# Kernel optimization log

Hardware: AMD Instinct MI355X
Metric: run time of the kernel (lower is better)

Reference implementation:

```python
import jax, jax.numpy as jnp
import numpy as np

D = 256  # input_dim


def setup_inputs() -> dict:
    key = jax.random.key(0)
    ks = jax.random.split(key, 10)
    s = 1.0 / np.sqrt(D)  # torch Linear init scale (uniform bound)
    desc0 = jax.random.normal(ks[0], (4, 4096, D), dtype=jnp.float32)
    desc1 = jax.random.normal(ks[1], (4, 4096, D), dtype=jnp.float32)
    def lin(kw, kb):
        W = jax.random.uniform(kw, (D, D), jnp.float32, -s, s)
        b = jax.random.uniform(kb, (D,), jnp.float32, -s, s)
        return W, b
    Wq, bq = lin(ks[2], ks[3])
    Wk, bk = lin(ks[4], ks[5])
    Wv, bv = lin(ks[6], ks[7])
    Wo, bo = lin(ks[8], ks[9])
    return {"desc0": desc0, "desc1": desc1,
            "Wq": Wq, "bq": bq, "Wk": Wk, "bk": bk,
            "Wv": Wv, "bv": bv, "Wo": Wo, "bo": bo}


def reference(desc0, desc1, Wq, bq, Wk, bk, Wv, bv, Wo, bo):
    # torch Linear: y = x @ W.T + b
    q = desc0 @ Wq.T + bq                      # [B, N0, D]
    k = desc1 @ Wk.T + bk                      # [B, N1, D]
    v = desc1 @ Wv.T + bv                      # [B, N1, D]
    scale = 1.0 / jnp.sqrt(jnp.asarray(q.shape[-1], q.dtype))
    attn = jnp.einsum('bqd,bkd->bqk', q, k) * scale  # [B, N0, N1]
    weights = jax.nn.softmax(attn, axis=-1)
    out = jnp.einsum('bqk,bkd->bqd', weights, v)     # [B, N0, D]
    return out @ Wo.T + bo
```

## Files before the change

### kernel.cpp

```cpp
#include <hip/hip_runtime.h>


typedef __attribute__((ext_vector_type(8))) __bf16 bf16x8;
typedef __attribute__((ext_vector_type(4))) float f32x4;
typedef __attribute__((ext_vector_type(16))) float f32x16;
typedef __attribute__((ext_vector_type(4))) unsigned int u32x4;
typedef __attribute__((ext_vector_type(2))) unsigned int u32x2;
typedef __attribute__((ext_vector_type(4))) unsigned short us16x4;

__device__ __forceinline__ unsigned short f2bf(float f) {
  unsigned u = __builtin_bit_cast(unsigned, f);
  u += 0x7FFFu + ((u >> 16) & 1u);
  return (unsigned short)(u >> 16);
}
__device__ __forceinline__ unsigned pk2(float a, float b) {
  return (unsigned)f2bf(a) | ((unsigned)f2bf(b) << 16);
}
__device__ __forceinline__ unsigned cvtpk(float lo, float hi) {
  unsigned r;
  asm("v_cvt_pk_bf16_f32 %0, %1, %2" : "=v"(r) : "v"(lo), "v"(hi));
  return r;
}
__device__ __forceinline__ float bf2f(unsigned short s) {
  return __builtin_bit_cast(float, ((unsigned)s) << 16);
}
__device__ __forceinline__ int swz4(int r) { return (r ^ (r >> 2)) & 3; }
__device__ __forceinline__ bf16x8 ldbf16(const void* p) {
  return __builtin_bit_cast(bf16x8, *(const u32x4*)p);
}
__device__ __forceinline__ f32x4 mfma16(bf16x8 a, bf16x8 b, f32x4 c) {
  return __builtin_amdgcn_mfma_f32_16x16x32_bf16(a, b, c, 0, 0, 0);
}
__device__ __forceinline__ f32x16 mfma32(bf16x8 a, bf16x8 b, f32x16 c) {
  return __builtin_amdgcn_mfma_f32_32x32x16_bf16(a, b, c, 0, 0, 0);
}
__device__ __forceinline__ void gld16(void* lds, const void* gsrc) {
  __builtin_amdgcn_global_load_lds(
      (const __attribute__((address_space(1))) unsigned int*)gsrc,
      (__attribute__((address_space(3))) unsigned int*)lds, 16, 0, 0);
}

template <int IN_BF16, int MODE>
__global__ __launch_bounds__(256, 4) void proj_k(const void* __restrict__ Ain,
                                                 const float* __restrict__ W,
                                                 const float* __restrict__ bias,
                                                 void* __restrict__ Cout) {
  __shared__ __align__(16) unsigned short Al[2][64 * 32];
  __shared__ __align__(16) unsigned short Wl[2][64 * 32];
  __shared__ float biasl[64];
  const int tid = threadIdx.x;
  const int w = tid >> 6, l = tid & 63, g = l >> 4, c = l & 15;
  const int mt = blockIdx.x & 255, nq = blockIdx.x >> 8;
  const int row0 = mt * 64, n0 = nq * 64;
  if (tid < 64) biasl[tid] = bias[n0 + tid];

  const int sr = tid >> 2, seg = tid & 3;
  const int ssw = swz4(sr);

  {
    if (IN_BF16) {
      const unsigned short* ap = (const unsigned short*)Ain + (size_t)(row0 + sr) * 256 + seg * 8;
      *(u32x4*)&Al[0][sr * 32 + ((seg ^ ssw) << 3)] = *(const u32x4*)ap;
    } else {
      const float* ap = (const float*)Ain + (size_t)(row0 + sr) * 256 + seg * 8;
      float4 x = *(const float4*)ap, y = *(const float4*)(ap + 4);
      u32x4 v; v[0] = pk2(x.x, x.y); v[1] = pk2(x.z, x.w); v[2] = pk2(y.x, y.y); v[3] = pk2(y.z, y.w);
      *(u32x4*)&Al[0][sr * 32 + ((seg ^ ssw) << 3)] = v;
    }
    const float* wp = W + (size_t)(n0 + sr) * 256 + seg * 8;
    float4 x = *(const float4*)wp, y = *(const float4*)(wp + 4);
    u32x4 v; v[0] = pk2(x.x, x.y); v[1] = pk2(x.z, x.w); v[2] = pk2(y.x, y.y); v[3] = pk2(y.z, y.w);
    *(u32x4*)&Wl[0][sr * 32 + ((seg ^ ssw) << 3)] = v;
  }
  __syncthreads();

  f32x4 acc[4];
#pragma unroll
  for (int jt = 0; jt < 4; ++jt) acc[jt] = (f32x4){0.f, 0.f, 0.f, 0.f};

#pragma unroll 1
  for (int ch = 0; ch < 8; ++ch) {
    const int cur = ch & 1;
    const bool pre = (ch + 1 < 8);
    float4 ax, ay, wx, wy; u32x4 abv;
    if (pre) {
      const int ko = (ch + 1) * 32 + seg * 8;
      if (IN_BF16) {
        abv = *(const u32x4*)((const unsigned short*)Ain + (size_t)(row0 + sr) * 256 + ko);
      } else {
        const float* ap = (const float*)Ain + (size_t)(row0 + sr) * 256 + ko;
        ax = *(const float4*)ap; ay = *(const float4*)(ap + 4);
      }
      const float* wp = W + (size_t)(n0 + sr) * 256 + ko;
      wx = *(const float4*)wp; wy = *(const float4*)(wp + 4);
    }
    const int ra = w * 16 + c;
    bf16x8 af = ldbf16(&Al[cur][ra * 32 + ((g ^ swz4(ra)) << 3)]);
#pragma unroll
    for (int jt = 0; jt < 4; ++jt) {
      const int j = jt * 16 + c;
      bf16x8 bfr = ldbf16(&Wl[cur][j * 32 + ((g ^ swz4(j)) << 3)]);
      acc[jt] = mfma16(af, bfr, acc[jt]);
    }
    if (pre) {
      u32x4 v;
      if (IN_BF16) v = abv;
      else { v[0] = pk2(ax.x, ax.y); v[1] = pk2(ax.z, ax.w); v[2] = pk2(ay.x, ay.y); v[3] = pk2(ay.z, ay.w); }
      *(u32x4*)&Al[1 - cur][sr * 32 + ((seg ^ ssw) << 3)] = v;
      u32x4 vw; vw[0] = pk2(wx.x, wx.y); vw[1] = pk2(wx.z, wx.w); vw[2] = pk2(wy.x, wy.y); vw[3] = pk2(wy.z, wy.w);
      *(u32x4*)&Wl[1 - cur][sr * 32 + ((seg ^ ssw) << 3)] = vw;
    }
    __syncthreads();
  }

#pragma unroll
  for (int jt = 0; jt < 4; ++jt) {
    const int col = n0 + jt * 16 + c;
    const float bv = biasl[jt * 16 + c];
    const int rloc = w * 16 + (g << 2);
    if (MODE == 0) {
      unsigned short* q = (unsigned short*)Cout;
#pragma unroll
      for (int r = 0; r < 4; ++r)
        q[(size_t)(row0 + rloc + r) * 256 + col] = f2bf(acc[jt][r] + bv);
    } else if (MODE == 1) {
      unsigned short* vt = (unsigned short*)Cout;
      const int n = row0 + rloc;
      const int b = n >> 12, nl = n & 4095;
      us16x4 pk;
      pk[0] = f2bf(acc[jt][0] + bv); pk[1] = f2bf(acc[jt][1] + bv);
      pk[2] = f2bf(acc[jt][2] + bv); pk[3] = f2bf(acc[jt][3] + bv);
      *(us16x4*)(vt + (size_t)b * 1048576 + (size_t)(nl >> 6) * 16384 + col * 64 + (nl & 63)) = pk;
    } else {
      float* o = (float*)Cout;
#pragma unroll
      for (int r = 0; r < 4; ++r)
        o[(size_t)(row0 + rloc + r) * 256 + col] = acc[jt][r] + bv;
    }
  }
}

template <int NS>
__global__ __launch_bounds__(512, 2) void attn_k(const unsigned short* __restrict__ qg,
                                                 const unsigned short* __restrict__ kg,
                                                 const unsigned short* __restrict__ vg,
                                                 unsigned short* __restrict__ part,
                                                 float* __restrict__ lw) {
  __shared__ __align__(16) unsigned char smem[148480];
  const int tid = threadIdx.x, w = tid >> 6, l = tid & 63;
  const int l31 = l & 31, h5 = l >> 5;
  const int qt = w >> 1, hf = w & 1;
  const int bid = blockIdx.x;
  const int b4 = bid & 3;
  const int s = (NS == 2) ? ((bid >> 2) & 1) : 0;
  const int qtl = (NS == 2) ? (bid >> 3) : (bid >> 2);
  const int q0 = qtl * 128;
  const int NT = (NS == 2) ? 32 : 64;

  const unsigned short* kb = kg + (size_t)b4 * 1048576 + (size_t)s * 524288;
  const unsigned short* vb = vg + (size_t)b4 * 1048576 + (size_t)s * 32 * 16384;

  bf16x8 qf[16];
  {
    const unsigned short* qp = qg + ((size_t)b4 * 4096 + q0 + qt * 32 + l31) * 256;
#pragma unroll
    for (int kst = 0; kst < 16; ++kst) qf[kst] = ldbf16(qp + kst * 16 + h5 * 8);
  }

  f32x16 o[4];
#pragma unroll
  for (int d = 0; d < 4; ++d)
#pragma unroll
    for (int r = 0; r < 16; ++r) o[d][r] = 0.f;
  float l_run = 0.f;

  int goffK[4], goffV[4];
#pragma unroll
  for (int i = 0; i < 4; ++i) {
    const int sl = i * 512 + tid;
    const int kk = sl >> 5, ch = sl & 31;
    goffK[i] = kk * 256 + ((ch ^ (kk & 31)) << 3);
    const int r = sl >> 4, p16 = sl & 15;
    const int x = p16 ^ (r & 15);
    goffV[i] = (2 * r + (x >> 3)) * 64 + ((x & 7) << 3);
  }
#define STAGE(buf, t1)                                                                   \
  {                                                                                      \
    const unsigned short* _ks = kb + (size_t)(t1) * 16384;                               \
    const unsigned short* _vs = vb + (size_t)(t1) * 16384;                               \
    _Pragma("unroll") for (int i = 0; i < 4; ++i)                                        \
        gld16(smem + (buf) * 32768 + i * 8192 + w * 1024, _ks + goffK[i]);               \
    _Pragma("unroll") for (int i = 0; i < 4; ++i)                                        \
        gld16(smem + 65536 + (buf) * 32768 + i * 8192 + w * 1024, _vs + goffV[i]);       \
  }

  STAGE(0, 0);
  __syncthreads();

  const float alpha = 0.09016844f;
  unsigned char* Pq = smem + 131072 + qt * 4096;
  const int kkr = hf * 32 + l31;

#pragma unroll 1
  for (int t = 0; t < NT; ++t) {
    const int cur = t & 1;
    if (t + 1 < NT) STAGE(1 - cur, t + 1);

    const unsigned char* Kc = smem + cur * 32768 + kkr * 512;
    f32x16 sa, sb;
#pragma unroll
    for (int r = 0; r < 16; ++r) { sa[r] = 0.f; sb[r] = 0.f; }
    __builtin_amdgcn_s_setprio(1);
#pragma unroll
    for (int kst = 0; kst < 16; ++kst) {
      bf16x8 kf = ldbf16(Kc + (((kst * 2 + h5) ^ l31) << 4));
      if (kst & 1) sb = mfma32(kf, qf[kst], sb);
      else         sa = mfma32(kf, qf[kst], sa);
    }
    __builtin_amdgcn_s_setprio(0);

    float p[16];
#pragma unroll
    for (int r = 0; r < 16; ++r) p[r] = exp2f((sa[r] + sb[r]) * alpha);
    float ls = ((p[0] + p[1]) + (p[2] + p[3])) + ((p[4] + p[5]) + (p[6] + p[7])) +
               (((p[8] + p[9]) + (p[10] + p[11])) + ((p[12] + p[13]) + (p[14] + p[15])));
    ls += __shfl_xor(ls, 32);
    l_run += ls;

    unsigned u[8];
#pragma unroll
    for (int i = 0; i < 8; ++i) u[i] = cvtpk(p[2 * i], p[2 * i + 1]);
#pragma unroll
    for (int j = 0; j < 4; ++j) {
      u32x2 dv; dv[0] = u[2 * j]; dv[1] = u[2 * j + 1];
      *(u32x2*)(Pq + l31 * 128 + (((j + 4 * hf) ^ (l31 & 7)) << 4) + h5 * 8) = dv;
    }

    asm volatile("s_waitcnt lgkmcnt(0)\n\ts_barrier" ::: "memory");
    __builtin_amdgcn_sched_barrier(0);

    bf16x8 pb[4];
#pragma unroll
    for (int kst = 0; kst < 4; ++kst)
      pb[kst] = ldbf16(Pq + l31 * 128 + (((kst * 2 + h5) ^ (l31 & 7)) << 4));
    const unsigned char* Vc = smem + 65536 + cur * 32768;
    __builtin_amdgcn_s_setprio(1);
#pragma unroll
    for (int dsub = 0; dsub < 4; ++dsub) {
      const int dm = hf * 128 + dsub * 32 + l31;
      const int r = dm >> 1;
      const unsigned char* Vr = Vc + r * 256;
      const int xb = (dm & 1) * 8;
#pragma unroll
      for (int kst = 0; kst < 4; ++kst) {
        bf16x8 vf = ldbf16(Vr + (((xb + kst * 2 + h5) ^ (r & 15)) << 4));
        o[dsub] = mfma32(vf, pb[kst], o[dsub]);
      }
    }
    __builtin_amdgcn_s_setprio(0);

    __syncthreads();
  }
#undef STAGE

  float* Lb = (float*)(smem + 147456);
  if (l < 32) Lb[(qt * 2 + hf) * 32 + l31] = l_run;
  __syncthreads();

  unsigned char* T = smem + w * 16384;
#pragma unroll
  for (int dsub = 0; dsub < 4; ++dsub)
#pragma unroll
    for (int rg = 0; rg < 4; ++rg) {
      f32x4 wv;
      wv[0] = o[dsub][4 * rg + 0]; wv[1] = o[dsub][4 * rg + 1];
      wv[2] = o[dsub][4 * rg + 2]; wv[3] = o[dsub][4 * rg + 3];
      const int d4 = dsub * 8 + rg * 2 + h5;
      *(f32x4*)(T + l31 * 512 + ((d4 ^ l31) << 4)) = wv;
    }
  asm volatile("s_waitcnt lgkmcnt(0)" ::: "memory");
  __builtin_amdgcn_sched_barrier(0);
  {
    const int q2 = l >> 1, dh = l & 1;
    unsigned short* op = part + (size_t)s * 4194304 +
                         ((size_t)b4 * 4096 + q0 + qt * 32 + q2) * 256 + hf * 128 + dh * 64;
#pragma unroll
    for (int jj = 0; jj < 8; ++jj) {
      f32x4 r0 = *(const f32x4*)(T + q2 * 512 + (((dh * 16 + 2 * jj) ^ q2) << 4));
      f32x4 r1 = *(const f32x4*)(T + q2 * 512 + (((dh * 16 + 2 * jj + 1) ^ q2) << 4));
      u32x4 ov;
      ov[0] = pk2(r0[0], r0[1]); ov[1] = pk2(r0[2], r0[3]);
      ov[2] = pk2(r1[0], r1[1]); ov[3] = pk2(r1[2], r1[3]);
      *(u32x4*)(op + jj * 8) = ov;
    }
  }
  if (hf == 0 && l < 32) {
    const float lt = Lb[(qt * 2) * 32 + l31] + Lb[(qt * 2 + 1) * 32 + l31];
    lw[(size_t)s * 16384 + (size_t)b4 * 4096 + q0 + qt * 32 + l31] = lt;
  }
}

__global__ __launch_bounds__(256, 8) void merge_k(unsigned short* __restrict__ part,
                                                  const float* __restrict__ lw, int ns) {
  const int idx = blockIdx.x * 256 + threadIdx.x;
  const int q = idx >> 5, d8 = (idx & 31) * 8;
  unsigned short* p0 = part + (size_t)q * 256 + d8;
  u32x4 a = *(const u32x4*)p0;
  float acc[8];
#pragma unroll
  for (int i = 0; i < 4; ++i) {
    acc[2 * i] = bf2f((unsigned short)(a[i] & 0xFFFF));
    acc[2 * i + 1] = bf2f((unsigned short)(a[i] >> 16));
  }
  float lt = lw[q];
  if (ns == 2) {
    u32x4 b = *(const u32x4*)(p0 + 4194304);
#pragma unroll
    for (int i = 0; i < 4; ++i) {
      acc[2 * i] += bf2f((unsigned short)(b[i] & 0xFFFF));
      acc[2 * i + 1] += bf2f((unsigned short)(b[i] >> 16));
    }
    lt += lw[16384 + q];
  }
  const float inv = 1.f / lt;
  u32x4 ov;
#pragma unroll
  for (int i = 0; i < 4; ++i) ov[i] = pk2(acc[2 * i] * inv, acc[2 * i + 1] * inv);
  *(u32x4*)p0 = ov;
}

extern "C" void kernel_launch(void* const* d_in, const int* in_sizes, int n_in,
                              void* d_out, int out_size, void* d_ws, size_t ws_size,
                              hipStream_t stream) {
  (void)in_sizes; (void)n_in; (void)out_size;
  const float* desc0 = (const float*)d_in[0];
  const float* desc1 = (const float*)d_in[1];
  const float* Wq = (const float*)d_in[2];
  const float* bq = (const float*)d_in[3];
  const float* Wk = (const float*)d_in[4];
  const float* bk = (const float*)d_in[5];
  const float* Wv = (const float*)d_in[6];
  const float* bv = (const float*)d_in[7];
  const float* Wo = (const float*)d_in[8];
  const float* bo = (const float*)d_in[9];

  unsigned char* ws = (unsigned char*)d_ws;
  unsigned short* qw = (unsigned short*)(ws);
  unsigned short* kw = (unsigned short*)(ws + 8388608);
  unsigned short* vw = (unsigned short*)(ws + 16777216);
  unsigned short* part = (unsigned short*)(ws + 25165824);
  float* lwp = (float*)(ws + 41943040);

  const bool two = (ws_size >= 42008576ull);

  proj_k<0, 0><<<1024, 256, 0, stream>>>(desc0, Wq, bq, qw);
  proj_k<0, 0><<<1024, 256, 0, stream>>>(desc1, Wk, bk, kw);
  proj_k<0, 1><<<1024, 256, 0, stream>>>(desc1, Wv, bv, vw);
  if (two) {
    attn_k<2><<<256, 512, 0, stream>>>(qw, kw, vw, part, lwp);
    merge_k<<<2048, 256, 0, stream>>>(part, lwp, 2);
  } else {
    lwp = (float*)(ws + 33554432);
    attn_k<1><<<128, 512, 0, stream>>>(qw, kw, vw, part, lwp);
    merge_k<<<2048, 256, 0, stream>>>(part, lwp, 1);
  }
  proj_k<1, 2><<<1024, 256, 0, stream>>>(part, Wo, bo, (float*)d_out);
}
```

Before: 135.4 us.

## Pre-swizzle K into MFMA fragment layout and load it directly to registers

The K projection now writes its output in a fragment-ordered layout, so each attention wave can load its K operands straight from global memory into registers. This drops K from shared memory: no LDS staging, no swizzled LDS reads, and a smaller LDS footprint. The next tile's K is prefetched into registers during the current iteration. In exchange each wave carries 16 extra vector registers of K, and the coalesced K load from global memory sits on the critical path, which could add register pressure or latency.

```diff
diff --git a/kernel.cpp b/kernel.cpp
--- a/kernel.cpp
+++ b/kernel.cpp
@@ -131,22 +131,32 @@
       pk[0] = f2bf(acc[jt][0] + bv); pk[1] = f2bf(acc[jt][1] + bv);
       pk[2] = f2bf(acc[jt][2] + bv); pk[3] = f2bf(acc[jt][3] + bv);
       *(us16x4*)(vt + (size_t)b * 1048576 + (size_t)(nl >> 6) * 16384 + col * 64 + (nl & 63)) = pk;
-    } else {
+    } else if (MODE == 2) {
       float* o = (float*)Cout;
 #pragma unroll
       for (int r = 0; r < 4; ++r)
         o[(size_t)(row0 + rloc + r) * 256 + col] = acc[jt][r] + bv;
+    } else {
+      unsigned short* kq = (unsigned short*)Cout;
+      const int kst = (n0 >> 4) + jt;
+      const int j = c & 7, hb = c >> 3;
+#pragma unroll
+      for (int r = 0; r < 4; ++r) {
+        const int n = row0 + rloc + r;
+        kq[(size_t)(n >> 5) * 8192 + kst * 512 + (((n & 31) + hb * 32) << 3) + j] =
+            f2bf(acc[jt][r] + bv);
+      }
     }
   }
 }
 
 template <int NS>
 __global__ __launch_bounds__(512, 2) void attn_k(const unsigned short* __restrict__ qg,
-                                                 const unsigned short* __restrict__ kg,
+                                                 const unsigned short* __restrict__ kfb,
                                                  const unsigned short* __restrict__ vg,
                                                  unsigned short* __restrict__ part,
                                                  float* __restrict__ lw) {
-  __shared__ __align__(16) unsigned char smem[148480];
+  __shared__ __align__(16) unsigned char smem[132096];
   const int tid = threadIdx.x, w = tid >> 6, l = tid & 63;
   const int l31 = l & 31, h5 = l >> 5;
   const int qt = w >> 1, hf = w & 1;
@@ -157,7 +167,7 @@
   const int q0 = qtl * 128;
   const int NT = (NS == 2) ? 32 : 64;
 
-  const unsigned short* kb = kg + (size_t)b4 * 1048576 + (size_t)s * 524288;
+  const unsigned short* kb = kfb + (size_t)b4 * 1048576 + (size_t)s * 524288;
   const unsigned short* vb = vg + (size_t)b4 * 1048576 + (size_t)s * 32 * 16384;
 
   bf16x8 qf[16];
@@ -174,48 +184,49 @@
     for (int r = 0; r < 16; ++r) o[d][r] = 0.f;
   float l_run = 0.f;
 
-  int goffK[4], goffV[4];
+  int goffV[4];
 #pragma unroll
   for (int i = 0; i < 4; ++i) {
     const int sl = i * 512 + tid;
-    const int kk = sl >> 5, ch = sl & 31;
-    goffK[i] = kk * 256 + ((ch ^ (kk & 31)) << 3);
     const int r = sl >> 4, p16 = sl & 15;
     const int x = p16 ^ (r & 15);
     goffV[i] = (2 * r + (x >> 3)) * 64 + ((x & 7) << 3);
   }
-#define STAGE(buf, t1)                                                                   \
-  {                                                                                      \
-    const unsigned short* _ks = kb + (size_t)(t1) * 16384;                               \
-    const unsigned short* _vs = vb + (size_t)(t1) * 16384;                               \
-    _Pragma("unroll") for (int i = 0; i < 4; ++i)                                        \
-        gld16(smem + (buf) * 32768 + i * 8192 + w * 1024, _ks + goffK[i]);               \
-    _Pragma("unroll") for (int i = 0; i < 4; ++i)                                        \
-        gld16(smem + 65536 + (buf) * 32768 + i * 8192 + w * 1024, _vs + goffV[i]);       \
-  }
-
-  STAGE(0, 0);
+#define STAGEV(buf, t1)                                                            \
+  {                                                                                \
+    const unsigned short* _vs = vb + (size_t)(t1) * 16384;                         \
+    _Pragma("unroll") for (int i = 0; i < 4; ++i)                                  \
+        gld16(smem + (buf) * 32768 + i * 8192 + w * 1024, _vs + goffV[i]);         \
+  }
+#define LOADK(dst, t1)                                                             \
+  {                                                                                \
+    const unsigned short* _tb = kb + (size_t)((t1) * 2 + hf) * 8192 + l * 8;       \
+    _Pragma("unroll") for (int kst = 0; kst < 16; ++kst)                           \
+        dst[kst] = *(const u32x4*)(_tb + kst * 512);                               \
+  }
+
+  u32x4 kf[16];
+  LOADK(kf, 0);
+  STAGEV(0, 0);
   __syncthreads();
 
   const float alpha = 0.09016844f;
-  unsigned char* Pq = smem + 131072 + qt * 4096;
-  const int kkr = hf * 32 + l31;
+  unsigned char* Pq = smem + 65536 + qt * 4096;
 
 #pragma unroll 1
   for (int t = 0; t < NT; ++t) {
     const int cur = t & 1;
-    if (t + 1 < NT) STAGE(1 - cur, t + 1);
-
-    const unsigned char* Kc = smem + cur * 32768 + kkr * 512;
+    if (t + 1 < NT) STAGEV(1 - cur, t + 1);
+
     f32x16 sa, sb;
 #pragma unroll
     for (int r = 0; r < 16; ++r) { sa[r] = 0.f; sb[r] = 0.f; }
     __builtin_amdgcn_s_setprio(1);
 #pragma unroll
     for (int kst = 0; kst < 16; ++kst) {
-      bf16x8 kf = ldbf16(Kc + (((kst * 2 + h5) ^ l31) << 4));
-      if (kst & 1) sb = mfma32(kf, qf[kst], sb);
-      else         sa = mfma32(kf, qf[kst], sa);
+      bf16x8 kfr = __builtin_bit_cast(bf16x8, kf[kst]);
+      if (kst & 1) sb = mfma32(kfr, qf[kst], sb);
+      else         sa = mfma32(kfr, qf[kst], sa);
     }
     __builtin_amdgcn_s_setprio(0);
 
@@ -236,6 +247,8 @@
       *(u32x2*)(Pq + l31 * 128 + (((j + 4 * hf) ^ (l31 & 7)) << 4) + h5 * 8) = dv;
     }
 
+    if (t + 1 < NT) LOADK(kf, t + 1);
+
     asm volatile("s_waitcnt lgkmcnt(0)\n\ts_barrier" ::: "memory");
     __builtin_amdgcn_sched_barrier(0);
 
@@ -243,7 +256,7 @@
 #pragma unroll
     for (int kst = 0; kst < 4; ++kst)
       pb[kst] = ldbf16(Pq + l31 * 128 + (((kst * 2 + h5) ^ (l31 & 7)) << 4));
-    const unsigned char* Vc = smem + 65536 + cur * 32768;
+    const unsigned char* Vc = smem + cur * 32768;
     __builtin_amdgcn_s_setprio(1);
 #pragma unroll
     for (int dsub = 0; dsub < 4; ++dsub) {
@@ -261,9 +274,10 @@
 
     __syncthreads();
   }
-#undef STAGE
-
-  float* Lb = (float*)(smem + 147456);
+#undef STAGEV
+#undef LOADK
+
+  float* Lb = (float*)(smem + 131072);
   if (l < 32) Lb[(qt * 2 + hf) * 32 + l31] = l_run;
   __syncthreads();
 
@@ -354,7 +368,7 @@
   const bool two = (ws_size >= 42008576ull);
 
   proj_k<0, 0><<<1024, 256, 0, stream>>>(desc0, Wq, bq, qw);
-  proj_k<0, 0><<<1024, 256, 0, stream>>>(desc1, Wk, bk, kw);
+  proj_k<0, 3><<<1024, 256, 0, stream>>>(desc1, Wk, bk, kw);
   proj_k<0, 1><<<1024, 256, 0, stream>>>(desc1, Wv, bv, vw);
   if (two) {
     attn_k<2><<<256, 512, 0, stream>>>(qw, kw, vw, part, lwp);
```

Result: slower. 141.1 us (+4.2%).

## Fuse split-merge normalization into output projection and rework PV tile mapping

Applied to the files above, without the earlier changes.

Removes the separate merge kernel. The output projection now reads both split partial outputs, adds them, divides by the summed softmax denominators, and packs to bf16 while loading its A tiles. The attention PV stage is remapped so each wave covers a 64-dim by 64-query tile: V fragments are loaded once and reused across two query sub-tiles, with matching changes to the epilogue layout. The intent is to save a launch plus a full read and write of the partial buffer, at the cost of extra per-chunk ALU work and a second load stream in the projection kernel.

```diff
diff --git a/kernel.cpp b/kernel.cpp
--- a/kernel.cpp
+++ b/kernel.cpp
@@ -40,11 +40,12 @@
       (__attribute__((address_space(3))) unsigned int*)lds, 16, 0, 0);
 }
 
-template <int IN_BF16, int MODE>
+template <int IN_MODE, int MODE>
 __global__ __launch_bounds__(256, 4) void proj_k(const void* __restrict__ Ain,
                                                  const float* __restrict__ W,
                                                  const float* __restrict__ bias,
-                                                 void* __restrict__ Cout) {
+                                                 void* __restrict__ Cout,
+                                                 const float* __restrict__ lwA) {
   __shared__ __align__(16) unsigned short Al[2][64 * 32];
   __shared__ __align__(16) unsigned short Wl[2][64 * 32];
   __shared__ float biasl[64];
@@ -57,10 +58,33 @@
   const int sr = tid >> 2, seg = tid & 3;
   const int ssw = swz4(sr);
 
+  float ainv = 1.f;
+  if (IN_MODE >= 2) {
+    const int grow = row0 + sr;
+    float lt = lwA[grow];
+    if (IN_MODE == 2) lt += lwA[16384 + grow];
+    ainv = 1.f / lt;
+  }
+
   {
-    if (IN_BF16) {
+    if (IN_MODE == 1) {
       const unsigned short* ap = (const unsigned short*)Ain + (size_t)(row0 + sr) * 256 + seg * 8;
       *(u32x4*)&Al[0][sr * 32 + ((seg ^ ssw) << 3)] = *(const u32x4*)ap;
+    } else if (IN_MODE >= 2) {
+      const unsigned short* ap = (const unsigned short*)Ain + (size_t)(row0 + sr) * 256 + seg * 8;
+      u32x4 a0 = *(const u32x4*)ap, v;
+      u32x4 a1 = (IN_MODE == 2) ? *(const u32x4*)(ap + 4194304) : a0;
+#pragma unroll
+      for (int i = 0; i < 4; ++i) {
+        float lo = bf2f((unsigned short)(a0[i] & 0xFFFF));
+        float hi = bf2f((unsigned short)(a0[i] >> 16));
+        if (IN_MODE == 2) {
+          lo += bf2f((unsigned short)(a1[i] & 0xFFFF));
+          hi += bf2f((unsigned short)(a1[i] >> 16));
+        }
+        v[i] = pk2(lo * ainv, hi * ainv);
+      }
+      *(u32x4*)&Al[0][sr * 32 + ((seg ^ ssw) << 3)] = v;
     } else {
       const float* ap = (const float*)Ain + (size_t)(row0 + sr) * 256 + seg * 8;
       float4 x = *(const float4*)ap, y = *(const float4*)(ap + 4);
@@ -82,11 +106,15 @@
   for (int ch = 0; ch < 8; ++ch) {
     const int cur = ch & 1;
     const bool pre = (ch + 1 < 8);
-    float4 ax, ay, wx, wy; u32x4 abv;
+    float4 ax, ay, wx, wy; u32x4 abv, abv2;
     if (pre) {
       const int ko = (ch + 1) * 32 + seg * 8;
-      if (IN_BF16) {
+      if (IN_MODE == 1) {
         abv = *(const u32x4*)((const unsigned short*)Ain + (size_t)(row0 + sr) * 256 + ko);
+      } else if (IN_MODE >= 2) {
+        const unsigned short* ap = (const unsigned short*)Ain + (size_t)(row0 + sr) * 256 + ko;
+        abv = *(const u32x4*)ap;
+        if (IN_MODE == 2) abv2 = *(const u32x4*)(ap + 4194304);
       } else {
         const float* ap = (const float*)Ain + (size_t)(row0 + sr) * 256 + ko;
         ax = *(const float4*)ap; ay = *(const float4*)(ap + 4);
@@ -104,8 +132,21 @@
     }
     if (pre) {
       u32x4 v;
-      if (IN_BF16) v = abv;
-      else { v[0] = pk2(ax.x, ax.y); v[1] = pk2(ax.z, ax.w); v[2] = pk2(ay.x, ay.y); v[3] = pk2(ay.z, ay.w); }
+      if (IN_MODE == 1) v = abv;
+      else if (IN_MODE >= 2) {
+#pragma unroll
+        for (int i = 0; i < 4; ++i) {
+          float lo = bf2f((unsigned short)(abv[i] & 0xFFFF));
+          float hi = bf2f((unsigned short)(abv[i] >> 16));
+          if (IN_MODE == 2) {
+            lo += bf2f((unsigned short)(abv2[i] & 0xFFFF));
+            hi += bf2f((unsigned short)(abv2[i] >> 16));
+          }
+          v[i] = pk2(lo * ainv, hi * ainv);
+        }
+      } else {
+        v[0] = pk2(ax.x, ax.y); v[1] = pk2(ax.z, ax.w); v[2] = pk2(ay.x, ay.y); v[3] = pk2(ay.z, ay.w);
+      }
       *(u32x4*)&Al[1 - cur][sr * 32 + ((seg ^ ssw) << 3)] = v;
       u32x4 vw; vw[0] = pk2(wx.x, wx.y); vw[1] = pk2(wx.z, wx.w); vw[2] = pk2(wy.x, wy.y); vw[3] = pk2(wy.z, wy.w);
       *(u32x4*)&Wl[1 - cur][sr * 32 + ((seg ^ ssw) << 3)] = vw;
@@ -150,6 +191,7 @@
   const int tid = threadIdx.x, w = tid >> 6, l = tid & 63;
   const int l31 = l & 31, h5 = l >> 5;
   const int qt = w >> 1, hf = w & 1;
+  const int dh = w >> 1, qh = w & 1;
   const int bid = blockIdx.x;
   const int b4 = bid & 3;
   const int s = (NS == 2) ? ((bid >> 2) & 1) : 0;
@@ -239,23 +281,31 @@
     asm volatile("s_waitcnt lgkmcnt(0)\n\ts_barrier" ::: "memory");
     __builtin_amdgcn_sched_barrier(0);
 
-    bf16x8 pb[4];
-#pragma unroll
-    for (int kst = 0; kst < 4; ++kst)
-      pb[kst] = ldbf16(Pq + l31 * 128 + (((kst * 2 + h5) ^ (l31 & 7)) << 4));
     const unsigned char* Vc = smem + 65536 + cur * 32768;
+    bf16x8 va[8];
+#pragma unroll
+    for (int dd = 0; dd < 2; ++dd) {
+      const int dm = dh * 64 + dd * 32 + l31;
+      const int rr = dm >> 1;
+      const unsigned char* Vr = Vc + rr * 256;
+      const int xb = (dm & 1) * 8;
+#pragma unroll
+      for (int kst = 0; kst < 4; ++kst)
+        va[dd * 4 + kst] = ldbf16(Vr + (((xb + kst * 2 + h5) ^ (rr & 15)) << 4));
+    }
     __builtin_amdgcn_s_setprio(1);
 #pragma unroll
-    for (int dsub = 0; dsub < 4; ++dsub) {
-      const int dm = hf * 128 + dsub * 32 + l31;
-      const int r = dm >> 1;
-      const unsigned char* Vr = Vc + r * 256;
-      const int xb = (dm & 1) * 8;
-#pragma unroll
-      for (int kst = 0; kst < 4; ++kst) {
-        bf16x8 vf = ldbf16(Vr + (((xb + kst * 2 + h5) ^ (r & 15)) << 4));
-        o[dsub] = mfma32(vf, pb[kst], o[dsub]);
-      }
+    for (int qq = 0; qq < 2; ++qq) {
+      const unsigned char* Pr = smem + 131072 + (qh * 2 + qq) * 4096;
+      bf16x8 pb[4];
+#pragma unroll
+      for (int kst = 0; kst < 4; ++kst)
+        pb[kst] = ldbf16(Pr + l31 * 128 + (((kst * 2 + h5) ^ (l31 & 7)) << 4));
+#pragma unroll
+      for (int dd = 0; dd < 2; ++dd)
+#pragma unroll
+        for (int kst = 0; kst < 4; ++kst)
+          o[dd * 2 + qq] = mfma32(va[dd * 4 + kst], pb[kst], o[dd * 2 + qq]);
     }
     __builtin_amdgcn_s_setprio(0);
 
@@ -269,64 +319,42 @@
 
   unsigned char* T = smem + w * 16384;
 #pragma unroll
-  for (int dsub = 0; dsub < 4; ++dsub)
-#pragma unroll
-    for (int rg = 0; rg < 4; ++rg) {
-      f32x4 wv;
-      wv[0] = o[dsub][4 * rg + 0]; wv[1] = o[dsub][4 * rg + 1];
-      wv[2] = o[dsub][4 * rg + 2]; wv[3] = o[dsub][4 * rg + 3];
-      const int d4 = dsub * 8 + rg * 2 + h5;
-      *(f32x4*)(T + l31 * 512 + ((d4 ^ l31) << 4)) = wv;
-    }
+  for (int dd = 0; dd < 2; ++dd)
+#pragma unroll
+    for (int qq = 0; qq < 2; ++qq)
+#pragma unroll
+      for (int rg = 0; rg < 4; ++rg) {
+        f32x4 wv;
+        wv[0] = o[dd * 2 + qq][4 * rg + 0]; wv[1] = o[dd * 2 + qq][4 * rg + 1];
+        wv[2] = o[dd * 2 + qq][4 * rg + 2]; wv[3] = o[dd * 2 + qq][4 * rg + 3];
+        const int qloc = qq * 32 + l31;
+        const int c16 = dd * 8 + rg * 2 + h5;
+        *(f32x4*)(T + qloc * 256 + ((c16 ^ (qloc & 15)) << 4)) = wv;
+      }
   asm volatile("s_waitcnt lgkmcnt(0)" ::: "memory");
   __builtin_amdgcn_sched_barrier(0);
   {
-    const int q2 = l >> 1, dh = l & 1;
+    const int qloc = l;
+    f32x4 rv[16];
+#pragma unroll
+    for (int c16 = 0; c16 < 16; ++c16)
+      rv[c16] = *(const f32x4*)(T + qloc * 256 + ((c16 ^ (qloc & 15)) << 4));
     unsigned short* op = part + (size_t)s * 4194304 +
-                         ((size_t)b4 * 4096 + q0 + qt * 32 + q2) * 256 + hf * 128 + dh * 64;
-#pragma unroll
-    for (int jj = 0; jj < 8; ++jj) {
-      f32x4 r0 = *(const f32x4*)(T + q2 * 512 + (((dh * 16 + 2 * jj) ^ q2) << 4));
-      f32x4 r1 = *(const f32x4*)(T + q2 * 512 + (((dh * 16 + 2 * jj + 1) ^ q2) << 4));
+                         ((size_t)b4 * 4096 + q0 + qh * 64 + qloc) * 256 + dh * 64;
+#pragma unroll
+    for (int i = 0; i < 8; ++i) {
       u32x4 ov;
-      ov[0] = pk2(r0[0], r0[1]); ov[1] = pk2(r0[2], r0[3]);
-      ov[2] = pk2(r1[0], r1[1]); ov[3] = pk2(r1[2], r1[3]);
-      *(u32x4*)(op + jj * 8) = ov;
+      ov[0] = pk2(rv[2 * i][0], rv[2 * i][1]);
+      ov[1] = pk2(rv[2 * i][2], rv[2 * i][3]);
+      ov[2] = pk2(rv[2 * i + 1][0], rv[2 * i + 1][1]);
+      ov[3] = pk2(rv[2 * i + 1][2], rv[2 * i + 1][3]);
+      *(u32x4*)(op + i * 8) = ov;
     }
   }
   if (hf == 0 && l < 32) {
     const float lt = Lb[(qt * 2) * 32 + l31] + Lb[(qt * 2 + 1) * 32 + l31];
     lw[(size_t)s * 16384 + (size_t)b4 * 4096 + q0 + qt * 32 + l31] = lt;
   }
-}
-
-__global__ __launch_bounds__(256, 8) void merge_k(unsigned short* __restrict__ part,
-                                                  const float* __restrict__ lw, int ns) {
-  const int idx = blockIdx.x * 256 + threadIdx.x;
-  const int q = idx >> 5, d8 = (idx & 31) * 8;
-  unsigned short* p0 = part + (size_t)q * 256 + d8;
-  u32x4 a = *(const u32x4*)p0;
-  float acc[8];
-#pragma unroll
-  for (int i = 0; i < 4; ++i) {
-    acc[2 * i] = bf2f((unsigned short)(a[i] & 0xFFFF));
-    acc[2 * i + 1] = bf2f((unsigned short)(a[i] >> 16));
-  }
-  float lt = lw[q];
-  if (ns == 2) {
-    u32x4 b = *(const u32x4*)(p0 + 4194304);
-#pragma unroll
-    for (int i = 0; i < 4; ++i) {
-      acc[2 * i] += bf2f((unsigned short)(b[i] & 0xFFFF));
-      acc[2 * i + 1] += bf2f((unsigned short)(b[i] >> 16));
-    }
-    lt += lw[16384 + q];
-  }
-  const float inv = 1.f / lt;
-  u32x4 ov;
-#pragma unroll
-  for (int i = 0; i < 4; ++i) ov[i] = pk2(acc[2 * i] * inv, acc[2 * i + 1] * inv);
-  *(u32x4*)p0 = ov;
 }
 
 extern "C" void kernel_launch(void* const* d_in, const int* in_sizes, int n_in,
@@ -353,16 +381,15 @@
 
   const bool two = (ws_size >= 42008576ull);
 
-  proj_k<0, 0><<<1024, 256, 0, stream>>>(desc0, Wq, bq, qw);
-  proj_k<0, 0><<<1024, 256, 0, stream>>>(desc1, Wk, bk, kw);
-  proj_k<0, 1><<<1024, 256, 0, stream>>>(desc1, Wv, bv, vw);
+  proj_k<0, 0><<<1024, 256, 0, stream>>>(desc0, Wq, bq, qw, nullptr);
+  proj_k<0, 0><<<1024, 256, 0, stream>>>(desc1, Wk, bk, kw, nullptr);
+  proj_k<0, 1><<<1024, 256, 0, stream>>>(desc1, Wv, bv, vw, nullptr);
   if (two) {
     attn_k<2><<<256, 512, 0, stream>>>(qw, kw, vw, part, lwp);
-    merge_k<<<2048, 256, 0, stream>>>(part, lwp, 2);
+    proj_k<2, 2><<<1024, 256, 0, stream>>>(part, Wo, bo, (float*)d_out, lwp);
   } else {
     lwp = (float*)(ws + 33554432);
     attn_k<1><<<128, 512, 0, stream>>>(qw, kw, vw, part, lwp);
-    merge_k<<<2048, 256, 0, stream>>>(part, lwp, 1);
-  }
-  proj_k<1, 2><<<1024, 256, 0, stream>>>(part, Wo, bo, (float*)d_out);
-}
+    proj_k<3, 2><<<1024, 256, 0, stream>>>(part, Wo, bo, (float*)d_out, lwp);
+  }
+}
```

Measured after the change: 132.5 us. 1.02x faster.
